# Optimization experiments

Hardware: AMD Instinct MI355X
Metric: run time of the kernel (lower is better)

## Reference

```python
import jax, jax.numpy as jnp
import numpy as np

B, S, D = 8, 1024, 1152
H = 16
HD = D // H
HID = int(D * 4.0)
LN_EPS = 1e-5


def layer_norm(x, w, b):
    m = jnp.mean(x, axis=-1, keepdims=True)
    v = jnp.mean(jnp.square(x - m), axis=-1, keepdims=True)
    return (x - m) * jax.lax.rsqrt(v + LN_EPS) * w + b


def modulate(x, shift, scale):
    # shift/scale: [B, D] broadcast over seq
    return x * (1.0 + scale[:, None, :]) + shift[:, None, :]


def setup_inputs() -> dict:
    key = jax.random.key(0)
    ks = jax.random.split(key, 16)
    s = 0.02
    return {
        "x": jax.random.normal(ks[0], (B, S, D), jnp.float32),
        "c": jax.random.normal(ks[1], (B, D), jnp.float32),
        "ln1_w": jnp.ones((D,), jnp.float32),
        "ln1_b": jnp.zeros((D,), jnp.float32),
        "wq": jax.random.normal(ks[2], (D, D), jnp.float32) * s,
        "wk": jax.random.normal(ks[3], (D, D), jnp.float32) * s,
        "wv": jax.random.normal(ks[4], (D, D), jnp.float32) * s,
        "wo": jax.random.normal(ks[5], (D, D), jnp.float32) * s,
        "wo_b": jnp.zeros((D,), jnp.float32),
        "ln2_w": jnp.ones((D,), jnp.float32),
        "ln2_b": jnp.zeros((D,), jnp.float32),
        "fc1_w": jax.random.normal(ks[6], (D, HID), jnp.float32) * s,
        "fc1_b": jnp.zeros((HID,), jnp.float32),
        "fc2_w": jax.random.normal(ks[7], (HID, D), jnp.float32) * s,
        "fc2_b": jnp.zeros((D,), jnp.float32),
        "ada_w": jax.random.normal(ks[8], (D, 6 * D), jnp.float32) * s,
        "ada_b": jnp.zeros((6 * D,), jnp.float32),
    }


def attention(x, wq, wk, wv, wo, wo_b):
    b, s, d = x.shape
    q = (x @ wq).reshape(b, s, H, HD).transpose(0, 2, 1, 3)  # [B,H,S,hd]
    k = (x @ wk).reshape(b, s, H, HD).transpose(0, 2, 1, 3)
    v = (x @ wv).reshape(b, s, H, HD).transpose(0, 2, 1, 3)
    scale = 1.0 / np.sqrt(HD).astype(np.float32)
    att = jnp.einsum("bhqd,bhkd->bhqk", q, k) * scale
    att = jax.nn.softmax(att, axis=-1)
    out = jnp.einsum("bhqk,bhkd->bhqd", att, v)
    out = out.transpose(0, 2, 1, 3).reshape(b, s, d)
    return out @ wo + wo_b


def reference(x, c, ln1_w, ln1_b, wq, wk, wv, wo, wo_b, ln2_w, ln2_b,
              fc1_w, fc1_b, fc2_w, fc2_b, ada_w, ada_b):
    mod = jax.nn.silu(c) @ ada_w + ada_b  # [B, 6D]
    sh_msa, sc_msa, g_msa, sh_mlp, sc_mlp, g_mlp = jnp.split(mod, 6, axis=1)
    h = modulate(layer_norm(x, ln1_w, ln1_b), sh_msa, sc_msa)
    x = x + g_msa[:, None, :] * attention(h, wq, wk, wv, wo, wo_b)
    h = modulate(layer_norm(x, ln2_w, ln2_b), sh_mlp, sc_mlp)
    h = jax.nn.gelu(h @ fc1_w + fc1_b, approximate=False) @ fc2_w + fc2_b
    x = x + g_mlp[:, None, :] * h
    return x
```

## Files before the change

### kernel.cpp

```cpp
#include <hip/hip_runtime.h>
#include <hip/hip_bf16.h>


typedef unsigned short u16;
typedef unsigned int u32;
typedef __attribute__((ext_vector_type(8))) short bf16x8;
typedef __attribute__((ext_vector_type(4))) float f32x4;

#define MFMA16(a, b, c) __builtin_amdgcn_mfma_f32_16x16x32_bf16((a), (b), (c), 0, 0, 0)

__device__ __forceinline__ u16 f2bf(float f) {
  __hip_bfloat16 h = __float2bfloat16(f);
  return __builtin_bit_cast(u16, h);
}

__device__ __forceinline__ void gload16(const u16* g, u16* l) {
  __builtin_amdgcn_global_load_lds(
      (const __attribute__((address_space(1))) unsigned int*)(const void*)g,
      (__attribute__((address_space(3))) unsigned int*)(void*)l, 16, 0, 0);
}

__global__ void k_silu(const float* __restrict__ c, float* __restrict__ o, int n) {
  int i = blockIdx.x * 256 + threadIdx.x;
  if (i < n) { float v = c[i]; o[i] = v / (1.f + __expf(-v)); }
}

__global__ __launch_bounds__(256) void k_modproj1(const float* __restrict__ sc,
                                                  const float* __restrict__ aw,
                                                  float* __restrict__ partial) {
  __shared__ float lc[8][144];
  int kc = blockIdx.y;
  for (int i = threadIdx.x; i < 1152; i += 256) {
    int b = i / 144, k = i % 144;
    lc[b][k] = sc[b * 1152 + kc * 144 + k];
  }
  __syncthreads();
  int j = blockIdx.x * 256 + threadIdx.x;
  float acc[8] = {0, 0, 0, 0, 0, 0, 0, 0};
  for (int k = 0; k < 144; ++k) {
    float w = aw[(size_t)(kc * 144 + k) * 6912 + j];
    #pragma unroll
    for (int b = 0; b < 8; ++b) acc[b] += lc[b][k] * w;
  }
  #pragma unroll
  for (int b = 0; b < 8; ++b) partial[((size_t)kc * 8 + b) * 6912 + j] = acc[b];
}

__global__ __launch_bounds__(256) void k_modproj2(const float* __restrict__ partial,
                                                  const float* __restrict__ ab,
                                                  float* __restrict__ mo) {
  int j = blockIdx.x * 256 + threadIdx.x;
  float bias = ab[j];
  #pragma unroll
  for (int b = 0; b < 8; ++b) {
    float s = 0.f;
    #pragma unroll
    for (int kc = 0; kc < 8; ++kc) s += partial[((size_t)kc * 8 + b) * 6912 + j];
    mo[(size_t)b * 6912 + j] = s + bias;
  }
}

__global__ __launch_bounds__(256) void k_tcvt(const float* __restrict__ in, u16* __restrict__ out,
                                              int K, int N) {
  __shared__ float t[32][33];
  int tx = threadIdx.x & 31, ty = threadIdx.x >> 5;
  size_t bx = (size_t)blockIdx.x * 32, by = (size_t)blockIdx.y * 32;
  #pragma unroll
  for (int i = 0; i < 4; ++i) t[ty + 8 * i][tx] = in[(by + ty + 8 * i) * N + bx + tx];
  __syncthreads();
  #pragma unroll
  for (int i = 0; i < 4; ++i) out[(bx + ty + 8 * i) * K + by + tx] = f2bf(t[tx][ty + 8 * i]);
}

__global__ __launch_bounds__(256) void k_lnmod(const float* __restrict__ xin,
                                               const float* __restrict__ w,
                                               const float* __restrict__ bs,
                                               const float* __restrict__ mo,
                                               int sh_off, int sc_off, u16* __restrict__ o) {
  int row = blockIdx.x;
  int b = row >> 10;
  int tid = threadIdx.x;
  const float4* x4 = (const float4*)(xin + (size_t)row * 1152);
  float4 v0 = x4[tid];
  float4 v1 = make_float4(0.f, 0.f, 0.f, 0.f);
  if (tid < 32) v1 = x4[256 + tid];
  float s = v0.x + v0.y + v0.z + v0.w + v1.x + v1.y + v1.z + v1.w;
  float sq = v0.x * v0.x + v0.y * v0.y + v0.z * v0.z + v0.w * v0.w +
             v1.x * v1.x + v1.y * v1.y + v1.z * v1.z + v1.w * v1.w;
  #pragma unroll
  for (int d = 32; d > 0; d >>= 1) { s += __shfl_down(s, d); sq += __shfl_down(sq, d); }
  __shared__ float ps[4], pq[4];
  int wid = tid >> 6, lane = tid & 63;
  if (lane == 0) { ps[wid] = s; pq[wid] = sq; }
  __syncthreads();
  float S = ps[0] + ps[1] + ps[2] + ps[3];
  float SQ = pq[0] + pq[1] + pq[2] + pq[3];
  float mean = S * (1.f / 1152.f);
  float var = SQ * (1.f / 1152.f) - mean * mean;
  float rs = rsqrtf(var + 1e-5f);
  const float* shp = mo + (size_t)b * 6912 + sh_off;
  const float* scp = mo + (size_t)b * 6912 + sc_off;
  u16* orow = o + (size_t)row * 1152;
  {
    int col = 4 * tid;
    ushort4 u; float y;
    y = (v0.x - mean) * rs * w[col + 0] + bs[col + 0]; u.x = f2bf(y * (1.f + scp[col + 0]) + shp[col + 0]);
    y = (v0.y - mean) * rs * w[col + 1] + bs[col + 1]; u.y = f2bf(y * (1.f + scp[col + 1]) + shp[col + 1]);
    y = (v0.z - mean) * rs * w[col + 2] + bs[col + 2]; u.z = f2bf(y * (1.f + scp[col + 2]) + shp[col + 2]);
    y = (v0.w - mean) * rs * w[col + 3] + bs[col + 3]; u.w = f2bf(y * (1.f + scp[col + 3]) + shp[col + 3]);
    *(ushort4*)&orow[col] = u;
  }
  if (tid < 32) {
    int col = 1024 + 4 * tid;
    ushort4 u; float y;
    y = (v1.x - mean) * rs * w[col + 0] + bs[col + 0]; u.x = f2bf(y * (1.f + scp[col + 0]) + shp[col + 0]);
    y = (v1.y - mean) * rs * w[col + 1] + bs[col + 1]; u.y = f2bf(y * (1.f + scp[col + 1]) + shp[col + 1]);
    y = (v1.z - mean) * rs * w[col + 2] + bs[col + 2]; u.z = f2bf(y * (1.f + scp[col + 2]) + shp[col + 2]);
    y = (v1.w - mean) * rs * w[col + 3] + bs[col + 3]; u.w = f2bf(y * (1.f + scp[col + 3]) + shp[col + 3]);
    *(ushort4*)&orow[col] = u;
  }
}

template <int EPI>
__global__ __launch_bounds__(256) void k_gemm(const u16* __restrict__ A, const u16* __restrict__ Bt,
                                              int Kst, int klen, u16* __restrict__ Cb,
                                              float* __restrict__ Cf,
                                              const float* __restrict__ bias,
                                              const float* __restrict__ res,
                                              const float* __restrict__ mo, int goff,
                                              u16* __restrict__ vt) {
  const int tid = threadIdx.x;
  const int w = tid >> 6, lane = tid & 63;
  const int wr = w >> 1, wc = w & 1;
  const int lr = lane & 15, kg = lane >> 4;

  const int nwg = gridDim.x * gridDim.y;
  const int id = blockIdx.y * gridDim.x + blockIdx.x;
  const int swz = (id & 7) * (nwg >> 3) + (id >> 3);
  const int tM = (swz / gridDim.x) * 128, tN = (swz % gridDim.x) * 128;
  const int N = gridDim.x * 128;
  const int koff = blockIdx.z * klen;

  __shared__ u16 lA[3][128 * 32];
  __shared__ u16 lB[3][128 * 32];
  f32x4 acc[4][4];
  #pragma unroll
  for (int m = 0; m < 4; ++m)
    #pragma unroll
    for (int n = 0; n < 4; ++n) acc[m][n] = f32x4{0.f, 0.f, 0.f, 0.f};

  const int lrow = lane >> 2, lseg = lane & 3;
  const int fl = (lrow & 3) ^ ((lrow >> 2) & 3);
  const u16* gA = A + (size_t)(tM + w * 32 + lrow) * Kst + (lseg ^ fl) * 8 + koff;
  const u16* gB = Bt + (size_t)(tN + w * 32 + lrow) * Kst + (lseg ^ fl) * 8 + koff;
  const size_t rstep = (size_t)16 * Kst;
  const int wo0 = (w * 32) * 32, wo1 = (w * 32 + 16) * 32;
  const int flane = (lr & 3) ^ ((lr >> 2) & 3);
  const int aoff = (wr * 64 + lr) * 32 + (kg ^ flane) * 8;
  const int boff = (wc * 64 + lr) * 32 + (kg ^ flane) * 8;

#define STAGE(buf, ks)                        \
  do {                                        \
    gload16(gA + (ks), lA[buf] + wo0);        \
    gload16(gA + rstep + (ks), lA[buf] + wo1);\
    gload16(gB + (ks), lB[buf] + wo0);        \
    gload16(gB + rstep + (ks), lB[buf] + wo1);\
  } while (0)

#define COMPUTE(buf)                                                                  \
  do {                                                                                \
    bf16x8 af[4], bfr[4];                                                             \
    _Pragma("unroll")                                                                 \
    for (int m = 0; m < 4; ++m) af[m] = *(const bf16x8*)&lA[buf][aoff + m * 16 * 32]; \
    _Pragma("unroll")                                                                 \
    for (int n = 0; n < 4; ++n) bfr[n] = *(const bf16x8*)&lB[buf][boff + n * 16 * 32];\
    _Pragma("unroll")                                                                 \
    for (int m = 0; m < 4; ++m)                                                       \
      _Pragma("unroll")                                                               \
      for (int n = 0; n < 4; ++n) acc[m][n] = MFMA16(af[m], bfr[n], acc[m][n]);       \
  } while (0)

#define WAITBAR(Nst)                                          \
  do {                                                        \
    asm volatile("s_waitcnt vmcnt(" #Nst ")" ::: "memory");   \
    __builtin_amdgcn_s_barrier();                             \
    __builtin_amdgcn_sched_barrier(0);                        \
  } while (0)

  const int nt = klen >> 5;
  STAGE(0, 0);
  STAGE(1, 32);
  int ks = 64;
  for (int g = 0; g < nt / 3 - 1; ++g) {
    WAITBAR(4); STAGE(2, ks);      COMPUTE(0);
    WAITBAR(4); STAGE(0, ks + 32); COMPUTE(1);
    WAITBAR(4); STAGE(1, ks + 64); COMPUTE(2);
    ks += 96;
  }
  WAITBAR(4); STAGE(2, ks); COMPUTE(0);
  WAITBAR(4); COMPUTE(1);
  WAITBAR(0); COMPUTE(2);
#undef STAGE
#undef COMPUTE
#undef WAITBAR

  if (EPI == 3) {
    #pragma unroll
    for (int m = 0; m < 4; ++m)
      #pragma unroll
      for (int n = 0; n < 4; ++n) {
        int gcol = tN + wc * 64 + n * 16 + lr;
        int s0 = tM + wr * 64 + m * 16 + kg * 4;
        if (tN < 2304) {
          #pragma unroll
          for (int r = 0; r < 4; ++r) Cb[(size_t)(s0 + r) * N + gcol] = f2bf(acc[m][n][r]);
        } else {
          int qq = gcol - 2304;
          int hh = qq / 72;
          int d = qq - hh * 72;
          int bb = s0 >> 10, sl = s0 & 1023;
          ushort4 u;
          u.x = f2bf(acc[m][n][0]); u.y = f2bf(acc[m][n][1]);
          u.z = f2bf(acc[m][n][2]); u.w = f2bf(acc[m][n][3]);
          *(ushort4*)&vt[(((size_t)bb * 16 + hh) * 72 + d) * 1024 + sl] = u;
        }
      }
  } else if (EPI == 4) {
    float* Po = Cf + (size_t)blockIdx.z * ((size_t)gridDim.y * 128) * N;
    #pragma unroll
    for (int m = 0; m < 4; ++m)
      #pragma unroll
      for (int n = 0; n < 4; ++n)
        #pragma unroll
        for (int r = 0; r < 4; ++r) {
          int grow = tM + wr * 64 + m * 16 + kg * 4 + r;
          int gcol = tN + wc * 64 + n * 16 + lr;
          Po[(size_t)grow * N + gcol] = acc[m][n][r];
        }
  } else {
    #pragma unroll
    for (int m = 0; m < 4; ++m)
      #pragma unroll
      for (int n = 0; n < 4; ++n)
        #pragma unroll
        for (int r = 0; r < 4; ++r) {
          int grow = tM + wr * 64 + m * 16 + kg * 4 + r;
          int gcol = tN + wc * 64 + n * 16 + lr;
          size_t idx = (size_t)grow * N + gcol;
          float v = acc[m][n][r];
          if (EPI == 1) {
            float g = mo[(size_t)(grow >> 10) * 6912 + goff + gcol];
            Cf[idx] = res[idx] + g * (v + bias[gcol]);
          } else {
            float z = v + bias[gcol];
            float z2 = z * z;
            float u = z * __fmaf_rn(z2, -0.0713548162f, -1.5957691216f);
            float e = __expf(u);
            float gel = z * __builtin_amdgcn_rcpf(1.f + e);
            Cb[idx] = f2bf(gel);
          }
        }
  }
}

__global__ __launch_bounds__(256) void k_fc2red(const float* __restrict__ p,
                                                const float* __restrict__ x1,
                                                const float* __restrict__ bias,
                                                const float* __restrict__ mo,
                                                float* __restrict__ out) {
  size_t i = ((size_t)blockIdx.x * 256 + threadIdx.x) * 4;
  int row = (int)(i / 1152);
  int col = (int)(i - (size_t)row * 1152);
  int b = row >> 10;
  float4 a0 = *(const float4*)(p + i);
  float4 a1 = *(const float4*)(p + 9437184ull + i);
  float4 r = *(const float4*)(x1 + i);
  const float* gp = mo + (size_t)b * 6912 + 5760 + col;
  const float* bp = bias + col;
  float4 o;
  o.x = r.x + gp[0] * (a0.x + a1.x + bp[0]);
  o.y = r.y + gp[1] * (a0.y + a1.y + bp[1]);
  o.z = r.z + gp[2] * (a0.z + a1.z + bp[2]);
  o.w = r.w + gp[3] * (a0.w + a1.w + bp[3]);
  *(float4*)(out + i) = o;
}

__global__ __launch_bounds__(256) void k_attn(const u16* __restrict__ QKV, const u16* __restrict__ Vt,
                                              u16* __restrict__ O) {
  const int tid = threadIdx.x;
  const int w = tid >> 6, lane = tid & 63;
  const int lr = lane & 15, kg = lane >> 4;
  int bx = blockIdx.x;
  bx = (bx & 7) * 256 + (bx >> 3);
  const int qt = bx & 15, h = (bx >> 4) & 15, b = bx >> 8;

  __shared__ u16 lQ[64][104];
  __shared__ u16 lK[64][104];
  __shared__ u16 lVt[80][72];
  __shared__ u16 lPt[4][16][72];

  const size_t qkbase = (size_t)b * 1024 * 3456 + (size_t)h * 72;
  const u16* Qg = QKV + qkbase;
  const u16* Kg = QKV + qkbase + 1152;
  const u16* Vg = Vt + ((size_t)(b * 16 + h) * 72) * 1024;

  const uint4 z4 = make_uint4(0, 0, 0, 0);
  for (int L = tid; L < 192; L += 256) {
    int r = L / 3, s = L - (L / 3) * 3;
    *(uint4*)&lQ[r][72 + s * 8] = z4;
    *(uint4*)&lK[r][72 + s * 8] = z4;
  }
  for (int L = tid; L < 72; L += 256) {
    int r = L / 9, s = L - (L / 9) * 9;
    *(uint4*)&lVt[72 + r][s * 8] = z4;
  }
  {
    int L = tid; int r = L / 9, s = L - r * 9;
    *(uint4*)&lQ[r][s * 8] = *(const uint4*)(Qg + (size_t)(qt * 64 + r) * 3456 + s * 8);
    L = tid + 256; r = L / 9; s = L - r * 9;
    *(uint4*)&lQ[r][s * 8] = *(const uint4*)(Qg + (size_t)(qt * 64 + r) * 3456 + s * 8);
    if (tid < 64) {
      L = tid + 512; r = L / 9; s = L - r * 9;
      *(uint4*)&lQ[r][s * 8] = *(const uint4*)(Qg + (size_t)(qt * 64 + r) * 3456 + s * 8);
    }
  }
  __syncthreads();

  bf16x8 bq[3];
  #pragma unroll
  for (int ks = 0; ks < 3; ++ks) bq[ks] = *(const bf16x8*)&lQ[w * 16 + lr][ks * 32 + kg * 8];

  const float scale = 0.11785113019775793f;
  float mrun = -1e30f, lrun = 0.f;
  f32x4 oacc[5];
  #pragma unroll
  for (int nd = 0; nd < 5; ++nd) oacc[nd] = f32x4{0.f, 0.f, 0.f, 0.f};

  for (int kt = 0; kt < 16; ++kt) {
    __syncthreads();
    {
      int L = tid; int r = L / 9, s = L - (L / 9) * 9;
      *(uint4*)&lK[r][s * 8] = *(const uint4*)(Kg + (size_t)(kt * 64 + r) * 3456 + s * 8);
      int d = tid >> 3, sg = tid & 7;
      *(uint4*)&lVt[d][sg * 8] = *(const uint4*)(Vg + (size_t)d * 1024 + kt * 64 + sg * 8);
      L = tid + 256; r = L / 9; s = L - r * 9;
      *(uint4*)&lK[r][s * 8] = *(const uint4*)(Kg + (size_t)(kt * 64 + r) * 3456 + s * 8);
      d = (tid + 256) >> 3; sg = tid & 7;
      *(uint4*)&lVt[d][sg * 8] = *(const uint4*)(Vg + (size_t)d * 1024 + kt * 64 + sg * 8);
      if (tid < 64) {
        L = tid + 512; r = L / 9; s = L - r * 9;
        *(uint4*)&lK[r][s * 8] = *(const uint4*)(Kg + (size_t)(kt * 64 + r) * 3456 + s * 8);
        d = (tid + 512) >> 3;
        *(uint4*)&lVt[d][sg * 8] = *(const uint4*)(Vg + (size_t)d * 1024 + kt * 64 + sg * 8);
      }
    }
    __syncthreads();

    f32x4 sfr[4];
    __builtin_amdgcn_s_setprio(1);
    #pragma unroll
    for (int kb = 0; kb < 4; ++kb) {
      f32x4 sv = f32x4{0.f, 0.f, 0.f, 0.f};
      #pragma unroll
      for (int ks = 0; ks < 3; ++ks) {
        bf16x8 ak = *(const bf16x8*)&lK[kb * 16 + lr][ks * 32 + kg * 8];
        sv = MFMA16(ak, bq[ks], sv);
      }
      sfr[kb] = sv;
    }
    __builtin_amdgcn_s_setprio(0);

    float mx = sfr[0][0];
    #pragma unroll
    for (int kb = 0; kb < 4; ++kb)
      #pragma unroll
      for (int r = 0; r < 4; ++r) mx = fmaxf(mx, sfr[kb][r]);
    mx = fmaxf(mx, __shfl_xor(mx, 16));
    mx = fmaxf(mx, __shfl_xor(mx, 32));
    mx *= scale;
    float mn = fmaxf(mrun, mx);
    float al = __expf(mrun - mn);
    mrun = mn;
    float sum = 0.f;
    #pragma unroll
    for (int kb = 0; kb < 4; ++kb) {
      #pragma unroll
      for (int rp = 0; rp < 2; ++rp) {
        float p0 = __expf(__fmaf_rn(sfr[kb][2 * rp], scale, -mn));
        float p1 = __expf(__fmaf_rn(sfr[kb][2 * rp + 1], scale, -mn));
        sum += p0 + p1;
        u32 pk = (u32)f2bf(p0) | ((u32)f2bf(p1) << 16);
        *(u32*)&lPt[w][lr][kb * 16 + kg * 4 + rp * 2] = pk;
      }
    }
    sum += __shfl_xor(sum, 16);
    sum += __shfl_xor(sum, 32);
    lrun = lrun * al + sum;
    #pragma unroll
    for (int nd = 0; nd < 5; ++nd)
      #pragma unroll
      for (int r = 0; r < 4; ++r) oacc[nd][r] *= al;

    __builtin_amdgcn_s_setprio(1);
    #pragma unroll
    for (int s = 0; s < 2; ++s) {
      bf16x8 bp = *(const bf16x8*)&lPt[w][lr][s * 32 + kg * 8];
      #pragma unroll
      for (int nd = 0; nd < 5; ++nd) {
        bf16x8 av = *(const bf16x8*)&lVt[nd * 16 + lr][s * 32 + kg * 8];
        oacc[nd] = MFMA16(av, bp, oacc[nd]);
      }
    }
    __builtin_amdgcn_s_setprio(0);
  }

  float inv = 1.f / lrun;
  size_t orow = ((size_t)b * 1024 + qt * 64 + w * 16 + lr) * 1152 + h * 72;
  #pragma unroll
  for (int nd = 0; nd < 5; ++nd) {
    int d0 = nd * 16 + kg * 4;
    if (d0 < 72) {
      ushort4 u;
      u.x = f2bf(oacc[nd][0] * inv);
      u.y = f2bf(oacc[nd][1] * inv);
      u.z = f2bf(oacc[nd][2] * inv);
      u.w = f2bf(oacc[nd][3] * inv);
      *(ushort4*)&O[orow + d0] = u;
    }
  }
}

extern "C" void kernel_launch(void* const* d_in, const int* in_sizes, int n_in,
                              void* d_out, int out_size, void* d_ws, size_t ws_size,
                              hipStream_t stream) {
  const float* x     = (const float*)d_in[0];
  const float* c     = (const float*)d_in[1];
  const float* ln1_w = (const float*)d_in[2];
  const float* ln1_b = (const float*)d_in[3];
  const float* wq    = (const float*)d_in[4];
  const float* wk    = (const float*)d_in[5];
  const float* wv    = (const float*)d_in[6];
  const float* wo    = (const float*)d_in[7];
  const float* wo_b  = (const float*)d_in[8];
  const float* ln2_w = (const float*)d_in[9];
  const float* ln2_b = (const float*)d_in[10];
  const float* fc1_w = (const float*)d_in[11];
  const float* fc1_b = (const float*)d_in[12];
  const float* fc2_w = (const float*)d_in[13];
  const float* fc2_b = (const float*)d_in[14];
  const float* ada_w = (const float*)d_in[15];
  const float* ada_b = (const float*)d_in[16];
  float* out = (float*)d_out;

  char* base = (char*)d_ws;
  size_t off = 0;
  auto alloc = [&](size_t nbytes) -> void* {
    void* p = base + off;
    off += (nbytes + 255) & ~(size_t)255;
    return p;
  };
  const size_t MD = 8192ull * 1152;
  float* silu_c = (float*)alloc(9216 * 4);
  float* partial = (float*)alloc(64ull * 6912 * 4);
  float* modb   = (float*)alloc(55296 * 4);
  u16* qkvT = (u16*)alloc(3456ull * 1152 * 2);
  u16* woT  = (u16*)alloc(1152ull * 1152 * 2);
  u16* fc1T = (u16*)alloc(4608ull * 1152 * 2);
  u16* fc2T = (u16*)alloc(1152ull * 4608 * 2);
  u16* hbuf = (u16*)alloc(MD * 2);
  float* x1 = (float*)alloc(MD * 4);
  u16* vtb  = (u16*)alloc(128ull * 72 * 1024 * 2);
  float* fc2p = (float*)alloc(2ull * MD * 4);
  u16* big  = (u16*)alloc(8192ull * 4608 * 2);
  u16* qkv = big;
  u16* m1 = big;

  k_silu<<<36, 256, 0, stream>>>(c, silu_c, 9216);
  k_modproj1<<<dim3(27, 8), 256, 0, stream>>>(silu_c, ada_w, partial);
  k_modproj2<<<27, 256, 0, stream>>>(partial, ada_b, modb);
  k_tcvt<<<dim3(36, 36), 256, 0, stream>>>(wq, qkvT, 1152, 1152);
  k_tcvt<<<dim3(36, 36), 256, 0, stream>>>(wk, qkvT + 1152ull * 1152, 1152, 1152);
  k_tcvt<<<dim3(36, 36), 256, 0, stream>>>(wv, qkvT + 2304ull * 1152, 1152, 1152);
  k_tcvt<<<dim3(36, 36), 256, 0, stream>>>(wo, woT, 1152, 1152);
  k_tcvt<<<dim3(144, 36), 256, 0, stream>>>(fc1_w, fc1T, 1152, 4608);
  k_tcvt<<<dim3(36, 144), 256, 0, stream>>>(fc2_w, fc2T, 4608, 1152);

  k_lnmod<<<8192, 256, 0, stream>>>(x, ln1_w, ln1_b, modb, 0, 1152, hbuf);
  k_gemm<3><<<dim3(27, 64), 256, 0, stream>>>(hbuf, qkvT, 1152, 1152, qkv, nullptr, nullptr, nullptr, nullptr, 0, vtb);
  k_attn<<<2048, 256, 0, stream>>>(qkv, vtb, hbuf);
  k_gemm<1><<<dim3(9, 64), 256, 0, stream>>>(hbuf, woT, 1152, 1152, nullptr, x1, wo_b, x, modb, 2304, nullptr);
  k_lnmod<<<8192, 256, 0, stream>>>(x1, ln2_w, ln2_b, modb, 3456, 4608, hbuf);
  k_gemm<2><<<dim3(36, 64), 256, 0, stream>>>(hbuf, fc1T, 1152, 1152, m1, nullptr, fc1_b, nullptr, nullptr, 0, nullptr);
  k_gemm<4><<<dim3(9, 64, 2), 256, 0, stream>>>(m1, fc2T, 4608, 2304, nullptr, fc2p, nullptr, nullptr, nullptr, 0, nullptr);
  k_fc2red<<<9216, 256, 0, stream>>>(fc2p, x1, fc2_b, modb, out);
}
```

Measured before the change: 615.0 us.

## Use 128x256 GEMM tiles for QKV/FC1/FC2 and bf16 split-K partials

Adds a wider-tile GEMM kernel (128x256 per block, each wave owning 128x64) for the QKV, FC1 and FC2 projections, padding the weight buffers to multiples of 256 columns. The aim is more MFMA work per LDS load and less operand traffic per output. FC2 split-K partials are now stored as bf16 with padded stride 1280 and summed in fp32 in the reduce kernel, halving that intermediate traffic. The cost is lower precision in the partial sums, more registers per thread, and wasted work on the padded columns. The padded weight rows are allocated but never written, so the extra outputs are either discarded or written to unused padded columns.

```diff
diff --git a/kernel.cpp b/kernel.cpp
--- a/kernel.cpp
+++ b/kernel.cpp
@@ -12,6 +12,11 @@
 __device__ __forceinline__ u16 f2bf(float f) {
   __hip_bfloat16 h = __float2bfloat16(f);
   return __builtin_bit_cast(u16, h);
+}
+
+__device__ __forceinline__ float bf2f(u16 u) {
+  u32 v = ((u32)u) << 16;
+  return __builtin_bit_cast(float, v);
 }
 
 __device__ __forceinline__ void gload16(const u16* g, u16* l) {
@@ -122,6 +127,125 @@
 }
 
 template <int EPI>
+__global__ __launch_bounds__(256) void k_gemmW(const u16* __restrict__ A, const u16* __restrict__ Bt,
+                                               int Kst, int klen, int NC,
+                                               u16* __restrict__ Cb, float* __restrict__ Cf,
+                                               const float* __restrict__ bias,
+                                               u16* __restrict__ vt) {
+  const int tid = threadIdx.x;
+  const int w = tid >> 6, lane = tid & 63;
+  const int lr = lane & 15, kg = lane >> 4;
+
+  const int nwg = gridDim.x * gridDim.y;
+  const int id = blockIdx.y * gridDim.x + blockIdx.x;
+  const int swz = (id & 7) * (nwg >> 3) + (id >> 3);
+  const int tM = (swz / gridDim.x) * 128, tN = (swz % gridDim.x) * 256;
+  const int koff = blockIdx.z * klen;
+
+  __shared__ u16 lA[3][128 * 32];
+  __shared__ u16 lB[3][256 * 32];
+  f32x4 acc[8][4];
+  #pragma unroll
+  for (int m = 0; m < 8; ++m)
+    #pragma unroll
+    for (int n = 0; n < 4; ++n) acc[m][n] = f32x4{0.f, 0.f, 0.f, 0.f};
+
+  const int lrow = lane >> 2, lseg = lane & 3;
+  const int fl = (lrow & 3) ^ ((lrow >> 2) & 3);
+  const u16* gA = A + (size_t)(tM + w * 32 + lrow) * Kst + (lseg ^ fl) * 8 + koff;
+  const u16* gB = Bt + (size_t)(tN + w * 64 + lrow) * Kst + (lseg ^ fl) * 8 + koff;
+  const size_t rstep = (size_t)16 * Kst;
+  const int a0 = (w * 32) * 32, a1 = (w * 32 + 16) * 32;
+  const int b0 = (w * 64) * 32, b1 = (w * 64 + 16) * 32, b2 = (w * 64 + 32) * 32, b3 = (w * 64 + 48) * 32;
+  const int flane = (lr & 3) ^ ((lr >> 2) & 3);
+  const int aoff = lr * 32 + (kg ^ flane) * 8;
+  const int boff = (w * 64 + lr) * 32 + (kg ^ flane) * 8;
+
+#define STAGE(buf, ks)                                 \
+  do {                                                 \
+    gload16(gA + (ks), lA[buf] + a0);                  \
+    gload16(gA + rstep + (ks), lA[buf] + a1);          \
+    gload16(gB + (ks), lB[buf] + b0);                  \
+    gload16(gB + rstep + (ks), lB[buf] + b1);          \
+    gload16(gB + 2 * rstep + (ks), lB[buf] + b2);      \
+    gload16(gB + 3 * rstep + (ks), lB[buf] + b3);      \
+  } while (0)
+
+#define COMPUTE(buf)                                                                   \
+  do {                                                                                 \
+    bf16x8 af[8], bfr[4];                                                              \
+    _Pragma("unroll")                                                                  \
+    for (int m = 0; m < 8; ++m) af[m] = *(const bf16x8*)&lA[buf][aoff + m * 16 * 32];  \
+    _Pragma("unroll")                                                                  \
+    for (int n = 0; n < 4; ++n) bfr[n] = *(const bf16x8*)&lB[buf][boff + n * 16 * 32]; \
+    _Pragma("unroll")                                                                  \
+    for (int m = 0; m < 8; ++m)                                                        \
+      _Pragma("unroll")                                                                \
+      for (int n = 0; n < 4; ++n) acc[m][n] = MFMA16(af[m], bfr[n], acc[m][n]);        \
+  } while (0)
+
+#define WAITBAR(Nst)                                          \
+  do {                                                        \
+    asm volatile("s_waitcnt vmcnt(" #Nst ")" ::: "memory");   \
+    __builtin_amdgcn_s_barrier();                             \
+    __builtin_amdgcn_sched_barrier(0);                        \
+  } while (0)
+
+  const int nt = klen >> 5;
+  STAGE(0, 0);
+  STAGE(1, 32);
+  int ks = 64;
+  for (int g = 0; g < nt / 3 - 1; ++g) {
+    WAITBAR(6); STAGE(2, ks);      COMPUTE(0);
+    WAITBAR(6); STAGE(0, ks + 32); COMPUTE(1);
+    WAITBAR(6); STAGE(1, ks + 64); COMPUTE(2);
+    ks += 96;
+  }
+  WAITBAR(6); STAGE(2, ks); COMPUTE(0);
+  WAITBAR(6); COMPUTE(1);
+  WAITBAR(0); COMPUTE(2);
+#undef STAGE
+#undef COMPUTE
+#undef WAITBAR
+
+  #pragma unroll
+  for (int m = 0; m < 8; ++m)
+    #pragma unroll
+    for (int n = 0; n < 4; ++n) {
+      int grow0 = tM + m * 16 + kg * 4;
+      int gcol = tN + w * 64 + n * 16 + lr;
+      if (EPI == 3) {
+        if (gcol < 2304) {
+          #pragma unroll
+          for (int r = 0; r < 4; ++r) Cb[(size_t)(grow0 + r) * 3456 + gcol] = f2bf(acc[m][n][r]);
+        } else if (gcol < 3456) {
+          int qq = gcol - 2304;
+          int hh = qq / 72;
+          int d = qq - hh * 72;
+          int bb = grow0 >> 10, sl = grow0 & 1023;
+          ushort4 u;
+          u.x = f2bf(acc[m][n][0]); u.y = f2bf(acc[m][n][1]);
+          u.z = f2bf(acc[m][n][2]); u.w = f2bf(acc[m][n][3]);
+          *(ushort4*)&vt[(((size_t)bb * 16 + hh) * 72 + d) * 1024 + sl] = u;
+        }
+      } else if (EPI == 5) {
+        u16* Po = Cb + (size_t)blockIdx.z * ((size_t)gridDim.y * 128) * NC;
+        #pragma unroll
+        for (int r = 0; r < 4; ++r) Po[(size_t)(grow0 + r) * NC + gcol] = f2bf(acc[m][n][r]);
+      } else {
+        #pragma unroll
+        for (int r = 0; r < 4; ++r) {
+          float z = acc[m][n][r] + bias[gcol];
+          float z2 = z * z;
+          float u = z * __fmaf_rn(z2, -0.0713548162f, -1.5957691216f);
+          float e = __expf(u);
+          Cb[(size_t)(grow0 + r) * NC + gcol] = f2bf(z * __builtin_amdgcn_rcpf(1.f + e));
+        }
+      }
+    }
+}
+
+template <int EPI>
 __global__ __launch_bounds__(256) void k_gemm(const u16* __restrict__ A, const u16* __restrict__ Bt,
                                               int Kst, int klen, u16* __restrict__ Cb,
                                               float* __restrict__ Cf,
@@ -204,66 +328,21 @@
 #undef COMPUTE
 #undef WAITBAR
 
-  if (EPI == 3) {
-    #pragma unroll
-    for (int m = 0; m < 4; ++m)
+  #pragma unroll
+  for (int m = 0; m < 4; ++m)
+    #pragma unroll
+    for (int n = 0; n < 4; ++n)
       #pragma unroll
-      for (int n = 0; n < 4; ++n) {
+      for (int r = 0; r < 4; ++r) {
+        int grow = tM + wr * 64 + m * 16 + kg * 4 + r;
         int gcol = tN + wc * 64 + n * 16 + lr;
-        int s0 = tM + wr * 64 + m * 16 + kg * 4;
-        if (tN < 2304) {
-          #pragma unroll
-          for (int r = 0; r < 4; ++r) Cb[(size_t)(s0 + r) * N + gcol] = f2bf(acc[m][n][r]);
-        } else {
-          int qq = gcol - 2304;
-          int hh = qq / 72;
-          int d = qq - hh * 72;
-          int bb = s0 >> 10, sl = s0 & 1023;
-          ushort4 u;
-          u.x = f2bf(acc[m][n][0]); u.y = f2bf(acc[m][n][1]);
-          u.z = f2bf(acc[m][n][2]); u.w = f2bf(acc[m][n][3]);
-          *(ushort4*)&vt[(((size_t)bb * 16 + hh) * 72 + d) * 1024 + sl] = u;
-        }
+        size_t idx = (size_t)grow * N + gcol;
+        float g = mo[(size_t)(grow >> 10) * 6912 + goff + gcol];
+        Cf[idx] = res[idx] + g * (acc[m][n][r] + bias[gcol]);
       }
-  } else if (EPI == 4) {
-    float* Po = Cf + (size_t)blockIdx.z * ((size_t)gridDim.y * 128) * N;
-    #pragma unroll
-    for (int m = 0; m < 4; ++m)
-      #pragma unroll
-      for (int n = 0; n < 4; ++n)
-        #pragma unroll
-        for (int r = 0; r < 4; ++r) {
-          int grow = tM + wr * 64 + m * 16 + kg * 4 + r;
-          int gcol = tN + wc * 64 + n * 16 + lr;
-          Po[(size_t)grow * N + gcol] = acc[m][n][r];
-        }
-  } else {
-    #pragma unroll
-    for (int m = 0; m < 4; ++m)
-      #pragma unroll
-      for (int n = 0; n < 4; ++n)
-        #pragma unroll
-        for (int r = 0; r < 4; ++r) {
-          int grow = tM + wr * 64 + m * 16 + kg * 4 + r;
-          int gcol = tN + wc * 64 + n * 16 + lr;
-          size_t idx = (size_t)grow * N + gcol;
-          float v = acc[m][n][r];
-          if (EPI == 1) {
-            float g = mo[(size_t)(grow >> 10) * 6912 + goff + gcol];
-            Cf[idx] = res[idx] + g * (v + bias[gcol]);
-          } else {
-            float z = v + bias[gcol];
-            float z2 = z * z;
-            float u = z * __fmaf_rn(z2, -0.0713548162f, -1.5957691216f);
-            float e = __expf(u);
-            float gel = z * __builtin_amdgcn_rcpf(1.f + e);
-            Cb[idx] = f2bf(gel);
-          }
-        }
-  }
-}
-
-__global__ __launch_bounds__(256) void k_fc2red(const float* __restrict__ p,
+}
+
+__global__ __launch_bounds__(256) void k_fc2red(const u16* __restrict__ p,
                                                 const float* __restrict__ x1,
                                                 const float* __restrict__ bias,
                                                 const float* __restrict__ mo,
@@ -272,16 +351,17 @@
   int row = (int)(i / 1152);
   int col = (int)(i - (size_t)row * 1152);
   int b = row >> 10;
-  float4 a0 = *(const float4*)(p + i);
-  float4 a1 = *(const float4*)(p + 9437184ull + i);
+  size_t pi = (size_t)row * 1280 + col;
+  ushort4 a0 = *(const ushort4*)(p + pi);
+  ushort4 a1 = *(const ushort4*)(p + 10485760ull + pi);
   float4 r = *(const float4*)(x1 + i);
   const float* gp = mo + (size_t)b * 6912 + 5760 + col;
   const float* bp = bias + col;
   float4 o;
-  o.x = r.x + gp[0] * (a0.x + a1.x + bp[0]);
-  o.y = r.y + gp[1] * (a0.y + a1.y + bp[1]);
-  o.z = r.z + gp[2] * (a0.z + a1.z + bp[2]);
-  o.w = r.w + gp[3] * (a0.w + a1.w + bp[3]);
+  o.x = r.x + gp[0] * (bf2f(a0.x) + bf2f(a1.x) + bp[0]);
+  o.y = r.y + gp[1] * (bf2f(a0.y) + bf2f(a1.y) + bp[1]);
+  o.z = r.z + gp[2] * (bf2f(a0.z) + bf2f(a1.z) + bp[2]);
+  o.w = r.w + gp[3] * (bf2f(a0.w) + bf2f(a1.w) + bp[3]);
   *(float4*)(out + i) = o;
 }
 
@@ -463,14 +543,14 @@
   float* silu_c = (float*)alloc(9216 * 4);
   float* partial = (float*)alloc(64ull * 6912 * 4);
   float* modb   = (float*)alloc(55296 * 4);
-  u16* qkvT = (u16*)alloc(3456ull * 1152 * 2);
+  u16* qkvT = (u16*)alloc(3584ull * 1152 * 2);
   u16* woT  = (u16*)alloc(1152ull * 1152 * 2);
   u16* fc1T = (u16*)alloc(4608ull * 1152 * 2);
-  u16* fc2T = (u16*)alloc(1152ull * 4608 * 2);
+  u16* fc2T = (u16*)alloc(1280ull * 4608 * 2);
   u16* hbuf = (u16*)alloc(MD * 2);
   float* x1 = (float*)alloc(MD * 4);
   u16* vtb  = (u16*)alloc(128ull * 72 * 1024 * 2);
-  float* fc2p = (float*)alloc(2ull * MD * 4);
+  u16* fc2p = (u16*)alloc(2ull * 8192 * 1280 * 2);
   u16* big  = (u16*)alloc(8192ull * 4608 * 2);
   u16* qkv = big;
   u16* m1 = big;
@@ -486,11 +566,11 @@
   k_tcvt<<<dim3(36, 144), 256, 0, stream>>>(fc2_w, fc2T, 4608, 1152);
 
   k_lnmod<<<8192, 256, 0, stream>>>(x, ln1_w, ln1_b, modb, 0, 1152, hbuf);
-  k_gemm<3><<<dim3(27, 64), 256, 0, stream>>>(hbuf, qkvT, 1152, 1152, qkv, nullptr, nullptr, nullptr, nullptr, 0, vtb);
+  k_gemmW<3><<<dim3(14, 64), 256, 0, stream>>>(hbuf, qkvT, 1152, 1152, 3456, qkv, nullptr, nullptr, vtb);
   k_attn<<<2048, 256, 0, stream>>>(qkv, vtb, hbuf);
   k_gemm<1><<<dim3(9, 64), 256, 0, stream>>>(hbuf, woT, 1152, 1152, nullptr, x1, wo_b, x, modb, 2304, nullptr);
   k_lnmod<<<8192, 256, 0, stream>>>(x1, ln2_w, ln2_b, modb, 3456, 4608, hbuf);
-  k_gemm<2><<<dim3(36, 64), 256, 0, stream>>>(hbuf, fc1T, 1152, 1152, m1, nullptr, fc1_b, nullptr, nullptr, 0, nullptr);
-  k_gemm<4><<<dim3(9, 64, 2), 256, 0, stream>>>(m1, fc2T, 4608, 2304, nullptr, fc2p, nullptr, nullptr, nullptr, 0, nullptr);
+  k_gemmW<2><<<dim3(18, 64), 256, 0, stream>>>(hbuf, fc1T, 1152, 1152, 4608, m1, nullptr, fc1_b, nullptr);
+  k_gemmW<5><<<dim3(5, 64, 2), 256, 0, stream>>>(m1, fc2T, 4608, 2304, 1280, fc2p, nullptr, nullptr, nullptr);
   k_fc2red<<<9216, 256, 0, stream>>>(fc2p, x1, fc2_b, modb, out);
 }
```

After: 852.2 us. 1.39x slower.
